# Optimization experiments

Measured on AMD Instinct MI355X. Metric: run time of the kernel, lower is better.

## Reference

```python
import jax, jax.numpy as jnp
import numpy as np


def _rope_tables(T, d):
    half = d // 2
    i = jnp.arange(half, dtype=jnp.float32)
    theta = 10000.0 ** (-2.0 * i / d)          # [half]
    m = jnp.arange(T, dtype=jnp.float32)[:, None]  # [T,1]
    ang = m * theta[None, :]                    # [T,half]
    return jnp.cos(ang), jnp.sin(ang)


def _rotate(v, cos, sin):
    # interleaved even/odd RoPE rotation, vectorized
    B, T, d = v.shape
    half = d // 2
    v2 = v.reshape(B, T, half, 2)
    even, odd = v2[..., 0], v2[..., 1]
    c = cos[None, :, :]
    s = sin[None, :, :]
    new_even = even * c - odd * s
    new_odd = even * s + odd * c
    return jnp.stack([new_even, new_odd], axis=-1).reshape(B, T, d)


def setup_inputs() -> dict:
    key = jax.random.key(0)
    k1, k2, k3, k4 = jax.random.split(key, 4)
    B, T, d = 4, 2048, 1024
    x = jax.random.normal(k1, (B, T, d), dtype=jnp.float32)
    scale = 0.02
    Wq = jax.random.normal(k2, (d, d), dtype=jnp.float32) * scale
    Wk = jax.random.normal(k3, (d, d), dtype=jnp.float32) * scale
    Wv = jax.random.normal(k4, (d, d), dtype=jnp.float32) * scale
    return {"x": x, "Wq": Wq, "Wk": Wk, "Wv": Wv}


def reference(x, Wq, Wk, Wv):
    B, T, d = x.shape
    cos, sin = _rope_tables(T, d)
    # torch Linear: y = x @ W.T
    Q = jnp.einsum('btd,ed->bte', x, Wq)
    K = jnp.einsum('btd,ed->bte', x, Wk)
    V = jnp.einsum('btd,ed->bte', x, Wv)
    Qr = _rotate(Q, cos, sin)
    Kr = _rotate(K, cos, sin)
    scores = jnp.einsum('bqd,bkd->bqk', Qr, Kr) / jnp.sqrt(jnp.float32(d))
    # NOTE: original uses tril with diagonal=1 (allows one future position)
    mask = jnp.tril(jnp.ones((T, T), dtype=bool), k=1)
    scores = jnp.where(mask[None, :, :], scores, -jnp.inf)
    attn = jax.nn.softmax(scores, axis=-1)
    out = jnp.einsum('bqk,bkd->bqd', attn, V)
    return out
```

## Files before the change

kernel.cpp:

```cpp
#include <hip/hip_runtime.h>


typedef float f32x4 __attribute__((ext_vector_type(4)));
typedef __bf16 bf16x8 __attribute__((ext_vector_type(8)));

#define BM 128
#define BN 128
#define BK 64

__device__ __forceinline__ unsigned short f2bf(float f) {
  union { float f; unsigned int u; } c; c.f = f;
  unsigned int u = c.u;
  u += 0x7fffu + ((u >> 16) & 1u);
  return (unsigned short)(u >> 16);
}
__device__ __forceinline__ float bf2f(unsigned short h) {
  union { unsigned int u; float f; } c; c.u = ((unsigned int)h) << 16;
  return c.f;
}

__device__ __forceinline__ void async16(const unsigned short* gp, unsigned short* lp) {
  __builtin_amdgcn_global_load_lds(
      (const __attribute__((address_space(1))) void*)gp,
      (__attribute__((address_space(3))) void*)lp, 16, 0, 0);
}

__global__ __launch_bounds__(256) void cvt_all(
    const float4* __restrict__ x, const float4* __restrict__ wq,
    const float4* __restrict__ wk, const float4* __restrict__ wv,
    ushort4* __restrict__ xb, ushort4* __restrict__ wb,
    float4* __restrict__ rowsums) {
  int b = blockIdx.x, t = threadIdx.x;
  if (b == 11264) {
#pragma unroll
    for (int i = 0; i < 8; ++i) rowsums[i * 256 + t] = float4{0.f, 0.f, 0.f, 0.f};
    return;
  }
  const float4* src;
  ushort4* dst;
  long i;
  if (b < 8192) { src = x; dst = xb; i = (long)b * 256 + t; }
  else if (b < 9216) { src = wq; dst = wb; i = (long)(b - 8192) * 256 + t; }
  else if (b < 10240) { src = wk; dst = wb + 262144; i = (long)(b - 9216) * 256 + t; }
  else { src = wv; dst = wb + 524288; i = (long)(b - 10240) * 256 + t; }
  float4 v = src[i];
  ushort4 o;
  o.x = f2bf(v.x); o.y = f2bf(v.y); o.z = f2bf(v.z); o.w = f2bf(v.w);
  dst[i] = o;
}

__device__ __forceinline__ void gemm_body(
    const unsigned short* __restrict__ A, const unsigned short* __restrict__ B,
    unsigned short* As, unsigned short* Bs,
    int lda, int ldb, int m0, int n0, int ktiles,
    int tid, int lane, int wave, f32x4 acc[4][4]) {
  const int wm = (wave >> 1) * 64;
  const int wn = (wave & 1) * 64;
  const int fm = lane & 15;
  const int q = lane >> 4;

  long goffA[4], goffB[4];
#pragma unroll
  for (int p = 0; p < 4; ++p) {
    int f = p * 256 + tid;
    int row = f >> 3;
    int c = (f & 7) ^ (row & 7);
    goffA[p] = (long)(m0 + row) * lda + c * 8;
    goffB[p] = (long)(n0 + row) * ldb + c * 8;
  }

  for (int kt = 0; kt < ktiles; ++kt) {
    const long k0 = (long)kt * BK;
    __syncthreads();
#pragma unroll
    for (int p = 0; p < 4; ++p) {
      async16(A + goffA[p] + k0, As + (p * 256 + tid) * 8);
      async16(B + goffB[p] + k0, Bs + (p * 256 + tid) * 8);
    }
    __syncthreads();

#pragma unroll
    for (int s = 0; s < 2; ++s) {
      bf16x8 af[4], bfr[4];
#pragma unroll
      for (int i = 0; i < 4; ++i) {
        int row = wm + i * 16 + fm;
        af[i] = *(const bf16x8*)&As[row * 64 + ((((s << 2) | q) ^ (row & 7)) << 3)];
      }
#pragma unroll
      for (int j = 0; j < 4; ++j) {
        int row = wn + j * 16 + fm;
        bfr[j] = *(const bf16x8*)&Bs[row * 64 + ((((s << 2) | q) ^ (row & 7)) << 3)];
      }
#pragma unroll
      for (int i = 0; i < 4; ++i)
#pragma unroll
        for (int j = 0; j < 4; ++j)
          acc[i][j] = __builtin_amdgcn_mfma_f32_16x16x32_bf16(af[i], bfr[j], acc[i][j], 0, 0, 0);
    }
  }
}

__global__ __launch_bounds__(256) void qkv_rope_gemm(
    const unsigned short* __restrict__ A, const unsigned short* __restrict__ B,
    unsigned short* __restrict__ Qr, unsigned short* __restrict__ Kr,
    unsigned short* __restrict__ Vt) {
  __shared__ __align__(16) unsigned short As[BM * BK];
  __shared__ __align__(16) unsigned short Bs[BN * BK];
  const int tid = threadIdx.x, lane = tid & 63, wave = tid >> 6;
  const int bm = blockIdx.x, bn = blockIdx.y;
  const int m0 = bm * BM, n0 = bn * BN;
  const int wm = (wave >> 1) * 64, wn = (wave & 1) * 64;
  const int q = lane >> 4, fm = lane & 15;

  f32x4 acc[4][4];
#pragma unroll
  for (int i = 0; i < 4; ++i)
#pragma unroll
    for (int j = 0; j < 4; ++j) acc[i][j] = (f32x4)(0.f);

  gemm_body(A, B, As, Bs, 1024, 1024, m0, n0, 16, tid, lane, wave, acc);

  if (n0 < 2048) {
    const float NEG = -13.287712379549449f / 1024.f;
    unsigned short* dst = (n0 < 1024) ? Qr : Kr;
    const int t00 = (m0 + wm + q * 4) & 2047;
#pragma unroll
    for (int j = 0; j < 4; ++j) {
      int c = (n0 & 1023) + wn + j * 16 + fm;
      float th = exp2f((float)(c & ~1) * NEG);
      float sgn = (c & 1) ? 1.f : -1.f;
      float ang0 = (float)t00 * th;
      float cb = __cosf(ang0), sb = __sinf(ang0);
      float c1 = __cosf(th), s1 = __sinf(th);
      float c16 = __cosf(16.f * th), s16 = __sinf(16.f * th);
#pragma unroll
      for (int i = 0; i < 4; ++i) {
        int gmB = m0 + wm + i * 16 + q * 4;
        float cr = cb, sr = sb;
#pragma unroll
        for (int r = 0; r < 4; ++r) {
          float v = acc[i][j][r];
          float p = __shfl_xor(v, 1);
          dst[(long)(gmB + r) * 1024 + c] = f2bf(v * cr + sgn * p * sr);
          float crn = cr * c1 - sr * s1;
          sr = sr * c1 + cr * s1;
          cr = crn;
        }
        float cbn = cb * c16 - sb * s16;
        sb = sb * c16 + cb * s16;
        cb = cbn;
      }
    }
  } else {
    const int c0 = n0 - 2048;
#pragma unroll
    for (int j = 0; j < 4; ++j) {
      int c = c0 + wn + j * 16 + fm;
#pragma unroll
      for (int i = 0; i < 4; ++i) {
        int gmB = m0 + wm + i * 16 + q * 4;
        int b = gmB >> 11, t = gmB & 2047;
        ushort4 pk;
        pk.x = f2bf(acc[i][j][0]);
        pk.y = f2bf(acc[i][j][1]);
        pk.z = f2bf(acc[i][j][2]);
        pk.w = f2bf(acc[i][j][3]);
        *(ushort4*)&Vt[((long)b * 1024 + c) * 2048 + t] = pk;
      }
    }
  }
}

__global__ __launch_bounds__(256) void s_gemm(
    const unsigned short* __restrict__ Qr, const unsigned short* __restrict__ Kr,
    unsigned short* __restrict__ Sb, float* __restrict__ rowsums) {
  __shared__ __align__(16) unsigned short As[BM * BK];
  __shared__ __align__(16) unsigned short Bs[BN * BK];
  const int tid = threadIdx.x, lane = tid & 63, wave = tid >> 6;
  const int bm = blockIdx.y, bn = blockIdx.x, z = blockIdx.z;
  if (bn > bm + 1) return;
  const unsigned short* A = Qr + (long)z * 2048 * 1024;
  const unsigned short* B = Kr + (long)z * 2048 * 1024;
  unsigned short* S = Sb + (long)z * 2048 * 2048;
  float* rs = rowsums + (long)z * 2048;
  const int m0 = bm * BM, n0 = bn * BN;
  const int wm = (wave >> 1) * 64, wn = (wave & 1) * 64;
  const int q = lane >> 4, fm = lane & 15;

  f32x4 acc[4][4];
#pragma unroll
  for (int i = 0; i < 4; ++i)
#pragma unroll
    for (int j = 0; j < 4; ++j) acc[i][j] = (f32x4)(0.f);

  gemm_body(A, B, As, Bs, 1024, 1024, m0, n0, 16, tid, lane, wave, acc);

  float* rsum = (float*)Bs;
  __syncthreads();
  if (tid < 128) rsum[tid] = 0.f;
  __syncthreads();

#pragma unroll
  for (int i = 0; i < 4; ++i) {
    int gmB = m0 + wm + i * 16 + q * 4;
    float ps[4] = {0.f, 0.f, 0.f, 0.f};
#pragma unroll
    for (int j = 0; j < 4; ++j) {
      int gn = n0 + wn + j * 16 + fm;
#pragma unroll
      for (int r = 0; r < 4; ++r) {
        float e = (gn <= gmB + r + 1) ? __expf(acc[i][j][r] * 0.03125f) : 0.f;
        unsigned short h = f2bf(e);
        S[(long)(gmB + r) * 2048 + gn] = h;
        ps[r] += bf2f(h);
      }
    }
#pragma unroll
    for (int r = 0; r < 4; ++r) {
      float v = ps[r];
      v += __shfl_xor(v, 1);
      v += __shfl_xor(v, 2);
      v += __shfl_xor(v, 4);
      v += __shfl_xor(v, 8);
      if (fm == 0) atomicAdd(&rsum[wm + i * 16 + q * 4 + r], v);
    }
  }
  __syncthreads();
  if (tid < 128) atomicAdd(&rs[m0 + tid], rsum[tid]);
}

__global__ __launch_bounds__(256) void pv_gemm(
    const unsigned short* __restrict__ Sb, const unsigned short* __restrict__ Vt,
    const float* __restrict__ rowsums, float* __restrict__ out, int b0) {
  __shared__ __align__(16) unsigned short As[BM * BK];
  __shared__ __align__(16) unsigned short Bs[BN * BK];
  const int tid = threadIdx.x, lane = tid & 63, wave = tid >> 6;
  const int bm = blockIdx.y, bn = blockIdx.x, z = blockIdx.z;
  const unsigned short* A = Sb + (long)z * 2048 * 2048;
  const unsigned short* B = Vt + (long)(b0 + z) * 1024 * 2048;
  const float* rs = rowsums + (long)(b0 + z) * 2048;
  float* C = out + (long)(b0 + z) * 2048 * 1024;
  int ktiles = 2 * bm + 3;
  if (ktiles > 32) ktiles = 32;
  const int m0 = bm * BM, n0 = bn * BN;
  const int wm = (wave >> 1) * 64, wn = (wave & 1) * 64;
  const int q = lane >> 4, fm = lane & 15;

  f32x4 acc[4][4];
#pragma unroll
  for (int i = 0; i < 4; ++i)
#pragma unroll
    for (int j = 0; j < 4; ++j) acc[i][j] = (f32x4)(0.f);

  gemm_body(A, B, As, Bs, 2048, 2048, m0, n0, ktiles, tid, lane, wave, acc);

#pragma unroll
  for (int i = 0; i < 4; ++i) {
    int gmB = m0 + wm + i * 16 + q * 4;
#pragma unroll
    for (int r = 0; r < 4; ++r) {
      float inv = 1.f / rs[gmB + r];
#pragma unroll
      for (int j = 0; j < 4; ++j) {
        int gn = n0 + wn + j * 16 + fm;
        C[(long)(gmB + r) * 1024 + gn] = acc[i][j][r] * inv;
      }
    }
  }
}

extern "C" void kernel_launch(void* const* d_in, const int* in_sizes, int n_in,
                              void* d_out, int out_size, void* d_ws, size_t ws_size,
                              hipStream_t stream) {
  const float* x = (const float*)d_in[0];
  const float* Wq = (const float*)d_in[1];
  const float* Wk = (const float*)d_in[2];
  const float* Wv = (const float*)d_in[3];
  float* out = (float*)d_out;

  float* rowsums = (float*)d_ws;
  unsigned short* Qr = (unsigned short*)d_ws + 16384;
  unsigned short* Kr = Qr + (long)8192 * 1024;
  unsigned short* Vt = Kr + (long)8192 * 1024;
  unsigned short* xb = Vt + (long)8192 * 1024;
  unsigned short* Wb = xb + (long)8192 * 1024;
  unsigned short* Sb = xb;

  int BCH = 4;
  while (BCH > 1 && (size_t)32768 + (size_t)(48 + 8 * BCH) * 1024 * 1024 > ws_size)
    BCH >>= 1;

  cvt_all<<<11265, 256, 0, stream>>>((const float4*)x, (const float4*)Wq,
                                     (const float4*)Wk, (const float4*)Wv,
                                     (ushort4*)xb, (ushort4*)Wb, (float4*)rowsums);

  qkv_rope_gemm<<<dim3(64, 24), 256, 0, stream>>>(xb, Wb, Qr, Kr, Vt);

  for (int b0 = 0; b0 < 4; b0 += BCH) {
    s_gemm<<<dim3(16, 16, BCH), 256, 0, stream>>>(Qr + (long)b0 * 2048 * 1024,
                                                  Kr + (long)b0 * 2048 * 1024,
                                                  Sb, rowsums + (long)b0 * 2048);
    pv_gemm<<<dim3(8, 16, BCH), 256, 0, stream>>>(Sb, Vt, rowsums, out, b0);
  }
}
```

Measured before the change: 252.7 us.

## Compact causal tile grid, reverse PV row order, add occupancy hints, simplify load addressing

```diff
diff --git a/kernel.cpp b/kernel.cpp
--- a/kernel.cpp
+++ b/kernel.cpp
@@ -58,24 +58,20 @@
   const int wn = (wave & 1) * 64;
   const int fm = lane & 15;
   const int q = lane >> 4;
-
-  long goffA[4], goffB[4];
-#pragma unroll
-  for (int p = 0; p < 4; ++p) {
-    int f = p * 256 + tid;
-    int row = f >> 3;
-    int c = (f & 7) ^ (row & 7);
-    goffA[p] = (long)(m0 + row) * lda + c * 8;
-    goffB[p] = (long)(n0 + row) * ldb + c * 8;
-  }
+  const int srow = tid >> 3;
+  const int c = (tid & 7) ^ (srow & 7);
+  const unsigned short* Ab = A + (long)(m0 + srow) * lda + c * 8;
+  const unsigned short* Bb = B + (long)(n0 + srow) * ldb + c * 8;
+  unsigned short* ldA = As + tid * 8;
+  unsigned short* ldB = Bs + tid * 8;
 
   for (int kt = 0; kt < ktiles; ++kt) {
     const long k0 = (long)kt * BK;
     __syncthreads();
 #pragma unroll
     for (int p = 0; p < 4; ++p) {
-      async16(A + goffA[p] + k0, As + (p * 256 + tid) * 8);
-      async16(B + goffB[p] + k0, Bs + (p * 256 + tid) * 8);
+      async16(Ab + (long)(p * 32) * lda + k0, ldA + p * 2048);
+      async16(Bb + (long)(p * 32) * ldb + k0, ldB + p * 2048);
     }
     __syncthreads();
 
@@ -101,7 +97,7 @@
   }
 }
 
-__global__ __launch_bounds__(256) void qkv_rope_gemm(
+__global__ __launch_bounds__(256, 3) void qkv_rope_gemm(
     const unsigned short* __restrict__ A, const unsigned short* __restrict__ B,
     unsigned short* __restrict__ Qr, unsigned short* __restrict__ Kr,
     unsigned short* __restrict__ Vt) {
@@ -172,14 +168,21 @@
   }
 }
 
-__global__ __launch_bounds__(256) void s_gemm(
+__global__ __launch_bounds__(256, 3) void s_gemm(
     const unsigned short* __restrict__ Qr, const unsigned short* __restrict__ Kr,
     unsigned short* __restrict__ Sb, float* __restrict__ rowsums) {
   __shared__ __align__(16) unsigned short As[BM * BK];
   __shared__ __align__(16) unsigned short Bs[BN * BK];
   const int tid = threadIdx.x, lane = tid & 63, wave = tid >> 6;
-  const int bm = blockIdx.y, bn = blockIdx.x, z = blockIdx.z;
-  if (bn > bm + 1) return;
+  const int z = blockIdx.z;
+  int idx = blockIdx.x, bm = 0;
+#pragma unroll 1
+  for (; bm < 16; ++bm) {
+    int cnt = (bm + 2 > 16) ? 16 : bm + 2;
+    if (idx < cnt) break;
+    idx -= cnt;
+  }
+  const int bn = idx;
   const unsigned short* A = Qr + (long)z * 2048 * 1024;
   const unsigned short* B = Kr + (long)z * 2048 * 1024;
   unsigned short* S = Sb + (long)z * 2048 * 2048;
@@ -230,13 +233,13 @@
   if (tid < 128) atomicAdd(&rs[m0 + tid], rsum[tid]);
 }
 
-__global__ __launch_bounds__(256) void pv_gemm(
+__global__ __launch_bounds__(256, 3) void pv_gemm(
     const unsigned short* __restrict__ Sb, const unsigned short* __restrict__ Vt,
     const float* __restrict__ rowsums, float* __restrict__ out, int b0) {
   __shared__ __align__(16) unsigned short As[BM * BK];
   __shared__ __align__(16) unsigned short Bs[BN * BK];
   const int tid = threadIdx.x, lane = tid & 63, wave = tid >> 6;
-  const int bm = blockIdx.y, bn = blockIdx.x, z = blockIdx.z;
+  const int bm = 15 - blockIdx.y, bn = blockIdx.x, z = blockIdx.z;
   const unsigned short* A = Sb + (long)z * 2048 * 2048;
   const unsigned short* B = Vt + (long)(b0 + z) * 1024 * 2048;
   const float* rs = rowsums + (long)(b0 + z) * 2048;
@@ -298,7 +301,7 @@
   qkv_rope_gemm<<<dim3(64, 24), 256, 0, stream>>>(xb, Wb, Qr, Kr, Vt);
 
   for (int b0 = 0; b0 < 4; b0 += BCH) {
-    s_gemm<<<dim3(16, 16, BCH), 256, 0, stream>>>(Qr + (long)b0 * 2048 * 1024,
+    s_gemm<<<dim3(151, 1, BCH), 256, 0, stream>>>(Qr + (long)b0 * 2048 * 1024,
                                                   Kr + (long)b0 * 2048 * 1024,
                                                   Sb, rowsums + (long)b0 * 2048);
     pv_gemm<<<dim3(8, 16, BCH), 256, 0, stream>>>(Sb, Vt, rowsums, out, b0);
```

Result: faster. 226.8 us (-10.3%).
